# Kernel tuning notes

Hardware: AMD Instinct MI355X
Metric: run time of the kernel (lower is better)

## Reference

```python
import jax, jax.numpy as jnp
import numpy as np

K = 3        # kernel_size
STRIDE = 1
PAD = 1
DIL = 1


def setup_inputs() -> dict:
    key = jax.random.key(0)
    ks = jax.random.split(key, 5)
    B, C, H, W, O = 4, 64, 128, 128, 64
    x = jax.random.normal(ks[0], (B, C, H, W), jnp.float32)
    # small offset-conv weights -> offsets of a few pixels (realistic trained regime)
    offset_w = jax.random.normal(ks[1], (2 * K * K, C, K, K), jnp.float32) * 0.01
    offset_b = jax.random.normal(ks[2], (2 * K * K,), jnp.float32) * 0.01
    weight = jax.random.normal(ks[3], (O, C, K, K), jnp.float32)
    bias = jax.random.normal(ks[4], (O,), jnp.float32)
    return {"x": x, "offset_w": offset_w, "offset_b": offset_b,
            "weight": weight, "bias": bias}


def _conv2d(x, w, b):
    y = jax.lax.conv_general_dilated(
        x, w, window_strides=(STRIDE, STRIDE),
        padding=[(PAD, PAD), (PAD, PAD)],
        dimension_numbers=("NCHW", "OIHW", "NCHW"))
    return y + b[None, :, None, None]


def _deform_conv2d(x, offset, weight, bias):
    B, C, H, W = x.shape
    O = weight.shape[0]
    KK = K * K
    Ho, Wo = offset.shape[2], offset.shape[3]
    # offset channels ordered (y, x) per kernel tap: [B, KK, 2, Ho, Wo]
    off = offset.reshape(B, KK, 2, Ho, Wo)
    kyy, kxx = jnp.meshgrid(jnp.arange(K) * DIL, jnp.arange(K) * DIL, indexing="ij")
    kyy = kyy.reshape(KK).astype(x.dtype)
    kxx = kxx.reshape(KK).astype(x.dtype)
    base_y = (jnp.arange(Ho) * STRIDE - PAD).astype(x.dtype)
    base_x = (jnp.arange(Wo) * STRIDE - PAD).astype(x.dtype)
    # sampling positions [B, KK, Ho, Wo]
    py = base_y[None, None, :, None] + kyy[None, :, None, None] + off[:, :, 0]
    px = base_x[None, None, None, :] + kxx[None, :, None, None] + off[:, :, 1]

    y0 = jnp.floor(py); x0 = jnp.floor(px)
    y1 = y0 + 1.0;      x1 = x0 + 1.0
    wy1 = py - y0; wy0 = 1.0 - wy1
    wx1 = px - x0; wx0 = 1.0 - wx1

    xf = x.reshape(B, C, H * W)

    def corner(yc, xc):
        valid = (yc >= 0) & (yc < H) & (xc >= 0) & (xc < W)  # zero padding outside
        idx = (jnp.clip(yc, 0, H - 1) * W + jnp.clip(xc, 0, W - 1)).astype(jnp.int32)
        g = jax.vmap(lambda xb, ib: xb[:, ib.reshape(-1)])(xf, idx)  # [B, C, KK*Ho*Wo]
        g = g.reshape(B, C, KK, Ho, Wo)
        return g * valid[:, None].astype(x.dtype)

    val = (corner(y0, x0) * (wy0 * wx0)[:, None]
         + corner(y0, x1) * (wy0 * wx1)[:, None]
         + corner(y1, x0) * (wy1 * wx0)[:, None]
         + corner(y1, x1) * (wy1 * wx1)[:, None])  # [B, C, KK, Ho, Wo]

    out = jnp.einsum("bckhw,ock->bohw", val, weight.reshape(O, C, KK))
    return out + bias[None, :, None, None]


def reference(x, offset_w, offset_b, weight, bias):
    offset = _conv2d(x, offset_w, offset_b)
    return _deform_conv2d(x, offset, weight, bias)
```

## Files before the change

### kernel.cpp

```cpp
#include <hip/hip_runtime.h>

#define B_   4
#define C_   64
#define O_   64
#define H_   128
#define W_   128
#define HW_  (H_ * W_)
#define KK_  9
#define M_   18

typedef short  short8  __attribute__((ext_vector_type(8)));
typedef float  floatx4 __attribute__((ext_vector_type(4)));
typedef float  float2v __attribute__((ext_vector_type(2)));
typedef unsigned int   uint4v   __attribute__((ext_vector_type(4)));
typedef unsigned short ushort8v __attribute__((ext_vector_type(8)));

static __device__ __forceinline__ unsigned short f2bf(float f) {
    unsigned int u = __float_as_uint(f);
    u += 0x7FFFu + ((u >> 16) & 1u);
    return (unsigned short)(u >> 16);
}
static __device__ __forceinline__ float2v bf2x(unsigned int q) {
    float2v r;
    r.x = __uint_as_float(q << 16);
    r.y = __uint_as_float(q & 0xFFFF0000u);
    return r;
}
static __device__ __forceinline__ float2v pk_mul(float2v a, float2v b) {
    float2v d;
    asm("v_pk_mul_f32 %0, %1, %2" : "=v"(d) : "v"(a), "v"(b));
    return d;
}
static __device__ __forceinline__ float2v pk_fma(float2v a, float2v b, float2v c) {
    float2v d;
    asm("v_pk_fma_f32 %0, %1, %2, %3" : "=v"(d) : "v"(a), "v"(b), "v"(c));
    return d;
}

__global__ __launch_bounds__(256) void prep(
        const float* __restrict__ x, const float* __restrict__ w,
        const float* __restrict__ ow, unsigned short* __restrict__ xT,
        unsigned short* __restrict__ wtbf, unsigned short* __restrict__ owtbf) {
    const int blk = blockIdx.x;
    if (blk < 1024) {
        __shared__ unsigned short T[64][70];
        const int tid  = threadIdx.x;
        const int half = blk & 1;
        const int y    = (blk >> 1) & (H_ - 1);
        const int b    = blk >> 8;
        const float* xby = x + (size_t)b * C_ * HW_ + y * W_ + half * 64;
        for (int i = tid; i < 64 * 64; i += 256) {
            const int c = i >> 6, xc = i & 63;
            T[xc][c] = f2bf(xby[(size_t)c * HW_ + xc]);
        }
        __syncthreads();
        unsigned short* dst = xT + ((size_t)b * HW_ + y * W_ + half * 64) * 64;
        for (int j = tid; j < 512; j += 256) {
            const int x8 = j >> 3, c8 = j & 7;
            uint4v pk;
            #pragma unroll
            for (int k = 0; k < 4; ++k)
                pk[k] = *(const unsigned int*)&T[x8][c8 * 8 + k * 2];
            *(uint4v*)&dst[x8 * 64 + c8 * 8] = pk;
        }
    } else if (blk < 1042) {
        const int i = (blk - 1024) * 256 + threadIdx.x;
        const int lane = i & 63, rest = i >> 6;
        const int ot = rest & 3, cks = rest >> 2;
        const int chunk = cks / 6, ks = cks % 6;
        const int o = ot * 16 + (lane & 15);
        const int kbase = chunk * 192 + ks * 32 + (lane >> 4) * 8;
        ushort8v pk;
        #pragma unroll
        for (int j = 0; j < 8; ++j) {
            const int k = kbase + j;
            pk[j] = f2bf(w[o * 576 + (k & 63) * 9 + (k >> 6)]);
        }
        *(ushort8v*)&wtbf[(size_t)i * 8] = pk;
    } else {
        const int i = (blk - 1042) * 256 + threadIdx.x;
        const int lane = i & 63, rest = i >> 6;
        const int tile = rest & 1, tks = rest >> 1;
        const int tap = tks >> 1, ks = tks & 1;
        const int m = tile * 16 + (lane & 15);
        const int cb = ks * 32 + (lane >> 4) * 8;
        ushort8v pk;
        #pragma unroll
        for (int j = 0; j < 8; ++j)
            pk[j] = (m < M_) ? f2bf(ow[m * 576 + (cb + j) * 9 + tap])
                             : (unsigned short)0;
        *(ushort8v*)&owtbf[(size_t)i * 8] = pk;
    }
}

__global__ __launch_bounds__(256, 4) void dcn_fused(
        const unsigned short* __restrict__ xT,
        const unsigned short* __restrict__ owtbf, const float* __restrict__ ob,
        const unsigned short* __restrict__ wtbf, const float* __restrict__ bias,
        float* __restrict__ out) {
    __shared__ union {
        unsigned short P[3][66][72];
        float ep[4][64][17];
    } u;
    __shared__ float offs[4][M_][16];

    const int tid    = threadIdx.x;
    const int lane   = tid & 63;
    const int wslot  = __builtin_amdgcn_readfirstlane(tid >> 6);
    const int lane15 = lane & 15;
    const int quad   = lane >> 4;

    const int g    = blockIdx.x;
    const int xcd  = g & 7;
    const int slot = g >> 3;
    const int ho   = xcd * 16 + (slot >> 3);
    const int b    = (slot >> 1) & 3;
    const int wo_base = (slot & 1) << 6;

    const unsigned short* xTb = xT + (size_t)b * HW_ * 64;

    #pragma unroll
    for (int ky = 0; ky < 3; ++ky) {
        const int y  = ho - 1 + ky;
        const bool yv = (unsigned)y < (unsigned)H_;
        const unsigned short* src = xTb + (size_t)y * W_ * 64;
        for (int j = tid; j < 66 * 8; j += 256) {
            const int r = j >> 3, c8 = j & 7;
            const int cx = wo_base + r - 1;
            ushort8v p0 = {0, 0, 0, 0, 0, 0, 0, 0};
            if (yv && (unsigned)cx < (unsigned)W_)
                p0 = *(const ushort8v*)&src[cx * 64 + c8 * 8];
            *(ushort8v*)&u.P[ky][r][c8 * 8] = p0;
        }
    }
    __syncthreads();

    floatx4 oa0 = (floatx4){0.f, 0.f, 0.f, 0.f};
    floatx4 oa1 = (floatx4){0.f, 0.f, 0.f, 0.f};
    {
        const int pxt = wslot;
        #pragma unroll
        for (int ky = 0; ky < 3; ++ky) {
            #pragma unroll
            for (int kx = 0; kx < 3; ++kx) {
                const int tap = ky * 3 + kx;
                #pragma unroll
                for (int ks = 0; ks < 2; ++ks) {
                    const int kk = ks * 32 + quad * 8;
                    const short8 af =
                        *(const short8*)&u.P[ky][pxt * 16 + lane15 + kx][kk];
                    const int fb = ((tap * 2 + ks) * 2) * 64 + lane;
                    const short8 bf0 = *(const short8*)&owtbf[(size_t)fb * 8];
                    const short8 bf1 =
                        *(const short8*)&owtbf[(size_t)(fb + 64) * 8];
                    oa0 = __builtin_amdgcn_mfma_f32_16x16x32_bf16(af, bf0, oa0, 0, 0, 0);
                    oa1 = __builtin_amdgcn_mfma_f32_16x16x32_bf16(af, bf1, oa1, 0, 0, 0);
                }
            }
        }
    }
    {
        const float ob0 = ob[lane15];
        #pragma unroll
        for (int r = 0; r < 4; ++r) oa0[r] += ob0;
        *(floatx4*)&offs[wslot][lane15][quad * 4] = oa0;
        if (lane15 < 2) {
            const float ob1 = ob[16 + lane15];
            #pragma unroll
            for (int r = 0; r < 4; ++r) oa1[r] += ob1;
            *(floatx4*)&offs[wslot][16 + lane15][quad * 4] = oa1;
        }
    }
    __syncthreads();

    const int pxg = wslot * 16 + lane15;
    floatx4 acc[4];
    #pragma unroll
    for (int t = 0; t < 4; ++t) acc[t] = (floatx4){0.f, 0.f, 0.f, 0.f};

    for (int chunk = 0; chunk < 3; ++chunk) {
        #pragma unroll
        for (int tl = 0; tl < 3; ++tl) {
            const int k  = chunk * 3 + tl;
            const int ky = k / 3, kx = k - ky * 3;
            const float offy = offs[wslot][2 * k][lane15];
            const float offx = offs[wslot][2 * k + 1][lane15];
            const float py  = (float)(ho - 1 + ky) + offy;
            const float pxx = (float)(wo_base - 1 + kx + pxg) + offx;
            const float fy = floorf(py), fx = floorf(pxx);
            const int y0 = (int)fy, x0 = (int)fx;
            const int y1 = y0 + 1,  x1 = x0 + 1;
            const float wy1 = py - fy,  wy0 = 1.f - wy1;
            const float wx1 = pxx - fx, wx0 = 1.f - wx1;
            const bool y0v = (unsigned)y0 < (unsigned)H_;
            const bool y1v = (unsigned)y1 < (unsigned)H_;
            const bool x0v = (unsigned)x0 < (unsigned)W_;
            const bool x1v = (unsigned)x1 < (unsigned)W_;
            const float w00 = (y0v && x0v) ? wy0 * wx0 : 0.f;
            const float w01 = (y0v && x1v) ? wy0 * wx1 : 0.f;
            const float w10 = (y1v && x0v) ? wy1 * wx0 : 0.f;
            const float w11 = (y1v && x1v) ? wy1 * wx1 : 0.f;
            const float2v w00_2 = {w00, w00};
            const float2v w01_2 = {w01, w01};
            const float2v w10_2 = {w10, w10};
            const float2v w11_2 = {w11, w11};
            const int ry0 = min(max(y0, 0), H_ - 1);
            const int ry1 = min(max(y1, 0), H_ - 1);
            const int cx0 = min(max(x0, 0), W_ - 1);
            const int cx1 = min(max(x1, 0), W_ - 1);
            const int a00 = (ry0 * W_ + cx0) * 64;
            const int a01 = (ry0 * W_ + cx1) * 64;
            const int a10 = (ry1 * W_ + cx0) * 64;
            const int a11 = (ry1 * W_ + cx1) * 64;
            #pragma unroll
            for (int chalf = 0; chalf < 2; ++chalf) {
                const unsigned short* xp = xTb + chalf * 32 + quad * 8;
                const uint4v q00 = *(const uint4v*)&xp[a00];
                const uint4v q01 = *(const uint4v*)&xp[a01];
                const uint4v q10 = *(const uint4v*)&xp[a10];
                const uint4v q11 = *(const uint4v*)&xp[a11];
                uint4v pw;
                #pragma unroll
                for (int j = 0; j < 4; ++j) {
                    float2v v = pk_mul(bf2x(q00[j]), w00_2);
                    v = pk_fma(bf2x(q01[j]), w01_2, v);
                    v = pk_fma(bf2x(q10[j]), w10_2, v);
                    v = pk_fma(bf2x(q11[j]), w11_2, v);
                    pw[j] = __builtin_amdgcn_perm(
                        __float_as_uint(v.y) + 0x8000u,
                        __float_as_uint(v.x) + 0x8000u,
                        0x07060302u);
                }
                const short8 af = *(const short8*)&pw;
                const int cks = k * 2 + chalf;
                const unsigned short* wb = wtbf + (size_t)cks * 2048 + lane * 8;
                #pragma unroll
                for (int t = 0; t < 4; ++t) {
                    const short8 bfrag = *(const short8*)&wb[(size_t)t * 512];
                    acc[t] = __builtin_amdgcn_mfma_f32_16x16x32_bf16(
                                 af, bfrag, acc[t], 0, 0, 0);
                }
            }
        }
    }

    float* epw = &u.ep[wslot][0][0];
    #pragma unroll
    for (int t = 0; t < 4; ++t)
        #pragma unroll
        for (int r = 0; r < 4; ++r)
            epw[(t * 16 + lane15) * 17 + quad * 4 + r] = acc[t][r];

    const int wo = wo_base + wslot * 16 + lane15;
    #pragma unroll
    for (int i = 0; i < 16; ++i) {
        const int o = i * 4 + quad;
        out[(size_t)(b * O_ + o) * HW_ + ho * W_ + wo] =
            epw[o * 17 + lane15] + bias[o];
    }
}

extern "C" void kernel_launch(void* const* d_in, const int* in_sizes, int n_in,
                              void* d_out, int out_size, void* d_ws, size_t ws_size,
                              hipStream_t stream) {
    const float* x    = (const float*)d_in[0];
    const float* ow   = (const float*)d_in[1];
    const float* ob   = (const float*)d_in[2];
    const float* w    = (const float*)d_in[3];
    const float* bias = (const float*)d_in[4];
    float* out = (float*)d_out;

    unsigned short* wtbf  = (unsigned short*)d_ws;
    unsigned short* owtbf = wtbf + 4608 * 8;
    unsigned short* xT    = owtbf + 2304 * 8;

    prep<<<1051, 256, 0, stream>>>(x, w, ow, xT, wtbf, owtbf);
    dcn_fused<<<B_ * H_ * (W_ / 64), 256, 0, stream>>>(xT, owtbf, ob, wtbf, bias, out);
}
```

Measured before the change: 125.8 us.

## Split kernel taps across two wave halves and use channel-grouped xT layout

Doubles the block to 512 threads so each pixel tile is handled by two waves that split the 9 deformable taps (even/odd), then reduce their accumulators through shared memory before the epilogue. The transposed input is also changed from 64-channel-contiguous pixels to four groups of 16 channels per pixel, so each gather touches a 32-byte segment in a separate plane. The aim is more waves in flight to hide gather latency and a different cache-line footprint per gather. In exchange it adds an extra LDS reduction with two barriers, and the offset conv runs on only half the waves while the other half sit idle.

```diff
diff --git a/kernel.cpp b/kernel.cpp
--- a/kernel.cpp
+++ b/kernel.cpp
@@ -54,14 +54,18 @@
             T[xc][c] = f2bf(xby[(size_t)c * HW_ + xc]);
         }
         __syncthreads();
-        unsigned short* dst = xT + ((size_t)b * HW_ + y * W_ + half * 64) * 64;
         for (int j = tid; j < 512; j += 256) {
             const int x8 = j >> 3, c8 = j & 7;
+            const int gq  = c8 >> 1;
+            const int sub = (c8 & 1) * 8;
             uint4v pk;
             #pragma unroll
             for (int k = 0; k < 4; ++k)
                 pk[k] = *(const unsigned int*)&T[x8][c8 * 8 + k * 2];
-            *(uint4v*)&dst[x8 * 64 + c8 * 8] = pk;
+            unsigned short* dst = xT
+                + ((size_t)(b * 4 + gq) * HW_ + y * W_ + half * 64 + x8) * 16
+                + sub;
+            *(uint4v*)dst = pk;
         }
     } else if (blk < 1042) {
         const int i = (blk - 1024) * 256 + threadIdx.x;
@@ -93,7 +97,7 @@
     }
 }
 
-__global__ __launch_bounds__(256, 4) void dcn_fused(
+__global__ __launch_bounds__(512, 8) void dcn_fused(
         const unsigned short* __restrict__ xT,
         const unsigned short* __restrict__ owtbf, const float* __restrict__ ob,
         const unsigned short* __restrict__ wtbf, const float* __restrict__ bias,
@@ -106,7 +110,9 @@
 
     const int tid    = threadIdx.x;
     const int lane   = tid & 63;
-    const int wslot  = __builtin_amdgcn_readfirstlane(tid >> 6);
+    const int ws     = __builtin_amdgcn_readfirstlane(tid >> 6);
+    const int p      = ws & 3;
+    const int h      = ws >> 2;
     const int lane15 = lane & 15;
     const int quad   = lane >> 4;
 
@@ -117,28 +123,28 @@
     const int b    = (slot >> 1) & 3;
     const int wo_base = (slot & 1) << 6;
 
-    const unsigned short* xTb = xT + (size_t)b * HW_ * 64;
+    const unsigned short* xTb = xT + (size_t)b * (4 * HW_ * 16);
 
     #pragma unroll
     for (int ky = 0; ky < 3; ++ky) {
         const int y  = ho - 1 + ky;
         const bool yv = (unsigned)y < (unsigned)H_;
-        const unsigned short* src = xTb + (size_t)y * W_ * 64;
-        for (int j = tid; j < 66 * 8; j += 256) {
+        for (int j = tid; j < 66 * 8; j += 512) {
             const int r = j >> 3, c8 = j & 7;
+            const int gq = c8 >> 1, sub = (c8 & 1) * 8;
             const int cx = wo_base + r - 1;
             ushort8v p0 = {0, 0, 0, 0, 0, 0, 0, 0};
             if (yv && (unsigned)cx < (unsigned)W_)
-                p0 = *(const ushort8v*)&src[cx * 64 + c8 * 8];
+                p0 = *(const ushort8v*)&xTb[(size_t)gq * (HW_ * 16)
+                                            + ((size_t)y * W_ + cx) * 16 + sub];
             *(ushort8v*)&u.P[ky][r][c8 * 8] = p0;
         }
     }
     __syncthreads();
 
-    floatx4 oa0 = (floatx4){0.f, 0.f, 0.f, 0.f};
-    floatx4 oa1 = (floatx4){0.f, 0.f, 0.f, 0.f};
-    {
-        const int pxt = wslot;
+    if (h == 0) {
+        floatx4 oa0 = (floatx4){0.f, 0.f, 0.f, 0.f};
+        floatx4 oa1 = (floatx4){0.f, 0.f, 0.f, 0.f};
         #pragma unroll
         for (int ky = 0; ky < 3; ++ky) {
             #pragma unroll
@@ -148,7 +154,7 @@
                 for (int ks = 0; ks < 2; ++ks) {
                     const int kk = ks * 32 + quad * 8;
                     const short8 af =
-                        *(const short8*)&u.P[ky][pxt * 16 + lane15 + kx][kk];
+                        *(const short8*)&u.P[ky][p * 16 + lane15 + kx][kk];
                     const int fb = ((tap * 2 + ks) * 2) * 64 + lane;
                     const short8 bf0 = *(const short8*)&owtbf[(size_t)fb * 8];
                     const short8 bf1 =
@@ -158,103 +164,111 @@
                 }
             }
         }
-    }
-    {
         const float ob0 = ob[lane15];
         #pragma unroll
         for (int r = 0; r < 4; ++r) oa0[r] += ob0;
-        *(floatx4*)&offs[wslot][lane15][quad * 4] = oa0;
+        *(floatx4*)&offs[p][lane15][quad * 4] = oa0;
         if (lane15 < 2) {
             const float ob1 = ob[16 + lane15];
             #pragma unroll
             for (int r = 0; r < 4; ++r) oa1[r] += ob1;
-            *(floatx4*)&offs[wslot][16 + lane15][quad * 4] = oa1;
-        }
-    }
-    __syncthreads();
-
-    const int pxg = wslot * 16 + lane15;
+            *(floatx4*)&offs[p][16 + lane15][quad * 4] = oa1;
+        }
+    }
+    __syncthreads();
+
+    const int pxg = p * 16 + lane15;
     floatx4 acc[4];
     #pragma unroll
     for (int t = 0; t < 4; ++t) acc[t] = (floatx4){0.f, 0.f, 0.f, 0.f};
 
-    for (int chunk = 0; chunk < 3; ++chunk) {
-        #pragma unroll
-        for (int tl = 0; tl < 3; ++tl) {
-            const int k  = chunk * 3 + tl;
-            const int ky = k / 3, kx = k - ky * 3;
-            const float offy = offs[wslot][2 * k][lane15];
-            const float offx = offs[wslot][2 * k + 1][lane15];
-            const float py  = (float)(ho - 1 + ky) + offy;
-            const float pxx = (float)(wo_base - 1 + kx + pxg) + offx;
-            const float fy = floorf(py), fx = floorf(pxx);
-            const int y0 = (int)fy, x0 = (int)fx;
-            const int y1 = y0 + 1,  x1 = x0 + 1;
-            const float wy1 = py - fy,  wy0 = 1.f - wy1;
-            const float wx1 = pxx - fx, wx0 = 1.f - wx1;
-            const bool y0v = (unsigned)y0 < (unsigned)H_;
-            const bool y1v = (unsigned)y1 < (unsigned)H_;
-            const bool x0v = (unsigned)x0 < (unsigned)W_;
-            const bool x1v = (unsigned)x1 < (unsigned)W_;
-            const float w00 = (y0v && x0v) ? wy0 * wx0 : 0.f;
-            const float w01 = (y0v && x1v) ? wy0 * wx1 : 0.f;
-            const float w10 = (y1v && x0v) ? wy1 * wx0 : 0.f;
-            const float w11 = (y1v && x1v) ? wy1 * wx1 : 0.f;
-            const float2v w00_2 = {w00, w00};
-            const float2v w01_2 = {w01, w01};
-            const float2v w10_2 = {w10, w10};
-            const float2v w11_2 = {w11, w11};
-            const int ry0 = min(max(y0, 0), H_ - 1);
-            const int ry1 = min(max(y1, 0), H_ - 1);
-            const int cx0 = min(max(x0, 0), W_ - 1);
-            const int cx1 = min(max(x1, 0), W_ - 1);
-            const int a00 = (ry0 * W_ + cx0) * 64;
-            const int a01 = (ry0 * W_ + cx1) * 64;
-            const int a10 = (ry1 * W_ + cx0) * 64;
-            const int a11 = (ry1 * W_ + cx1) * 64;
-            #pragma unroll
-            for (int chalf = 0; chalf < 2; ++chalf) {
-                const unsigned short* xp = xTb + chalf * 32 + quad * 8;
-                const uint4v q00 = *(const uint4v*)&xp[a00];
-                const uint4v q01 = *(const uint4v*)&xp[a01];
-                const uint4v q10 = *(const uint4v*)&xp[a10];
-                const uint4v q11 = *(const uint4v*)&xp[a11];
-                uint4v pw;
-                #pragma unroll
-                for (int j = 0; j < 4; ++j) {
-                    float2v v = pk_mul(bf2x(q00[j]), w00_2);
-                    v = pk_fma(bf2x(q01[j]), w01_2, v);
-                    v = pk_fma(bf2x(q10[j]), w10_2, v);
-                    v = pk_fma(bf2x(q11[j]), w11_2, v);
-                    pw[j] = __builtin_amdgcn_perm(
-                        __float_as_uint(v.y) + 0x8000u,
-                        __float_as_uint(v.x) + 0x8000u,
-                        0x07060302u);
-                }
-                const short8 af = *(const short8*)&pw;
-                const int cks = k * 2 + chalf;
-                const unsigned short* wb = wtbf + (size_t)cks * 2048 + lane * 8;
-                #pragma unroll
-                for (int t = 0; t < 4; ++t) {
-                    const short8 bfrag = *(const short8*)&wb[(size_t)t * 512];
-                    acc[t] = __builtin_amdgcn_mfma_f32_16x16x32_bf16(
-                                 af, bfrag, acc[t], 0, 0, 0);
-                }
+    #pragma unroll 2
+    for (int k = h; k < 9; k += 2) {
+        const int ky = k / 3, kx = k - ky * 3;
+        const float offy = offs[p][2 * k][lane15];
+        const float offx = offs[p][2 * k + 1][lane15];
+        const float py  = (float)(ho - 1 + ky) + offy;
+        const float pxx = (float)(wo_base - 1 + kx + pxg) + offx;
+        const float fy = floorf(py), fx = floorf(pxx);
+        const int y0 = (int)fy, x0 = (int)fx;
+        const int y1 = y0 + 1,  x1 = x0 + 1;
+        const float wy1 = py - fy,  wy0 = 1.f - wy1;
+        const float wx1 = pxx - fx, wx0 = 1.f - wx1;
+        const bool y0v = (unsigned)y0 < (unsigned)H_;
+        const bool y1v = (unsigned)y1 < (unsigned)H_;
+        const bool x0v = (unsigned)x0 < (unsigned)W_;
+        const bool x1v = (unsigned)x1 < (unsigned)W_;
+        const float w00 = (y0v && x0v) ? wy0 * wx0 : 0.f;
+        const float w01 = (y0v && x1v) ? wy0 * wx1 : 0.f;
+        const float w10 = (y1v && x0v) ? wy1 * wx0 : 0.f;
+        const float w11 = (y1v && x1v) ? wy1 * wx1 : 0.f;
+        const float2v w00_2 = {w00, w00};
+        const float2v w01_2 = {w01, w01};
+        const float2v w10_2 = {w10, w10};
+        const float2v w11_2 = {w11, w11};
+        const int ry0 = min(max(y0, 0), H_ - 1);
+        const int ry1 = min(max(y1, 0), H_ - 1);
+        const int cx0 = min(max(x0, 0), W_ - 1);
+        const int cx1 = min(max(x1, 0), W_ - 1);
+        const int a00 = (ry0 * W_ + cx0) * 16;
+        const int a01 = (ry0 * W_ + cx1) * 16;
+        const int a10 = (ry1 * W_ + cx0) * 16;
+        const int a11 = (ry1 * W_ + cx1) * 16;
+        #pragma unroll
+        for (int chalf = 0; chalf < 2; ++chalf) {
+            const int c0 = chalf * 32 + quad * 8;
+            const unsigned short* xp =
+                xTb + (size_t)(c0 >> 4) * (HW_ * 16) + (c0 & 8);
+            const uint4v q00 = *(const uint4v*)&xp[a00];
+            const uint4v q01 = *(const uint4v*)&xp[a01];
+            const uint4v q10 = *(const uint4v*)&xp[a10];
+            const uint4v q11 = *(const uint4v*)&xp[a11];
+            uint4v pw;
+            #pragma unroll
+            for (int j = 0; j < 4; ++j) {
+                float2v v = pk_mul(bf2x(q00[j]), w00_2);
+                v = pk_fma(bf2x(q01[j]), w01_2, v);
+                v = pk_fma(bf2x(q10[j]), w10_2, v);
+                v = pk_fma(bf2x(q11[j]), w11_2, v);
+                pw[j] = __builtin_amdgcn_perm(
+                    __float_as_uint(v.y) + 0x8000u,
+                    __float_as_uint(v.x) + 0x8000u,
+                    0x07060302u);
             }
-        }
-    }
-
-    float* epw = &u.ep[wslot][0][0];
+            const short8 af = *(const short8*)&pw;
+            const int cks = k * 2 + chalf;
+            const unsigned short* wb = wtbf + (size_t)cks * 2048 + lane * 8;
+            #pragma unroll
+            for (int t = 0; t < 4; ++t) {
+                const short8 bfrag = *(const short8*)&wb[(size_t)t * 512];
+                acc[t] = __builtin_amdgcn_mfma_f32_16x16x32_bf16(
+                             af, bfrag, acc[t], 0, 0, 0);
+            }
+        }
+    }
+
+    float* epw = &u.ep[p][0][0];
+    if (h == 1) {
+        #pragma unroll
+        for (int t = 0; t < 4; ++t)
+            #pragma unroll
+            for (int r = 0; r < 4; ++r)
+                epw[(t * 16 + lane15) * 17 + quad * 4 + r] = acc[t][r];
+    }
+    __syncthreads();
+    if (h == 0) {
+        #pragma unroll
+        for (int t = 0; t < 4; ++t)
+            #pragma unroll
+            for (int r = 0; r < 4; ++r)
+                epw[(t * 16 + lane15) * 17 + quad * 4 + r] += acc[t][r];
+    }
+    __syncthreads();
+
+    const int wo = wo_base + p * 16 + lane15;
     #pragma unroll
-    for (int t = 0; t < 4; ++t)
-        #pragma unroll
-        for (int r = 0; r < 4; ++r)
-            epw[(t * 16 + lane15) * 17 + quad * 4 + r] = acc[t][r];
-
-    const int wo = wo_base + wslot * 16 + lane15;
-    #pragma unroll
-    for (int i = 0; i < 16; ++i) {
-        const int o = i * 4 + quad;
+    for (int i = 0; i < 8; ++i) {
+        const int o = (h * 8 + i) * 4 + quad;
         out[(size_t)(b * O_ + o) * HW_ + ho * W_ + wo] =
             epw[o * 17 + lane15] + bias[o];
     }
@@ -275,5 +289,5 @@
     unsigned short* xT    = owtbf + 2304 * 8;
 
     prep<<<1051, 256, 0, stream>>>(x, w, ow, xT, wtbf, owtbf);
-    dcn_fused<<<B_ * H_ * (W_ / 64), 256, 0, stream>>>(xT, owtbf, ob, wtbf, bias, out);
-}
+    dcn_fused<<<B_ * H_ * (W_ / 64), 512, 0, stream>>>(xT, owtbf, ob, wtbf, bias, out);
+}
```

New measurement: 110.7 us. -12.0%, faster.
